# Kernel optimization log

Measured on AMD Instinct MI355X. Metric: run time of the kernel, lower is better.

The kernel has to match this reference:

```python
import jax, jax.numpy as jnp
import numpy as np

D_MODEL = 1024
D_STATE = 16
D_CONV = 4
EXPAND = 2
INNER = EXPAND * D_MODEL          # 2048
DT_RANK = (D_MODEL + 15) // 16     # 64 ('auto' heuristic)
BATCH = 1
SEQLEN = 2048
DT_MIN, DT_MAX, DT_FLOOR = 1e-3, 1e-1, 1e-4


def setup_inputs() -> dict:
    key = jax.random.key(0)
    ks = jax.random.split(key, 8)
    hidden_states = jax.random.normal(ks[0], (BATCH, SEQLEN, D_MODEL), jnp.float32)
    W_in = jax.random.normal(ks[1], (2 * INNER, D_MODEL), jnp.float32) * (D_MODEL ** -0.5)
    conv_w = jax.random.normal(ks[2], (INNER, D_CONV), jnp.float32) * 0.02
    conv_b = jnp.zeros((INNER,), jnp.float32)
    W_x = jax.random.normal(ks[3], (DT_RANK + 2 * D_STATE, INNER), jnp.float32) * (INNER ** -0.5)
    dt_init_std = DT_RANK ** -0.5
    W_dt = jax.random.uniform(ks[4], (INNER, DT_RANK), jnp.float32, -dt_init_std, dt_init_std)
    # dt_bias = inverse-softplus of dt sampled log-uniform in [dt_min, dt_max]
    dt = jnp.exp(jax.random.uniform(ks[5], (INNER,), jnp.float32)
                 * (np.log(DT_MAX) - np.log(DT_MIN)) + np.log(DT_MIN))
    dt = jnp.clip(dt, DT_FLOOR)
    dt_bias = dt + jnp.log(-jnp.expm1(-dt))
    A_log = jax.random.normal(ks[6], (INNER, D_STATE), jnp.float32) * 0.5
    D_skip = jnp.ones((INNER,), jnp.float32)
    W_out = jax.random.normal(ks[7], (D_MODEL, INNER), jnp.float32) * (INNER ** -0.5)
    return dict(hidden_states=hidden_states, W_in=W_in, conv_w=conv_w, conv_b=conv_b,
                W_x=W_x, W_dt=W_dt, dt_bias=dt_bias, A_log=A_log, D_skip=D_skip, W_out=W_out)


def _silu(x):
    return x * jax.nn.sigmoid(x)


def reference(hidden_states, W_in, conv_w, conv_b, W_x, W_dt, dt_bias, A_log, D_skip, W_out):
    # in_proj: (B, L, d_model) -> (B, L, 2*inner), split into x-branch and gate
    xz = hidden_states @ W_in.T
    proj, gate = jnp.split(xz, 2, axis=-1)

    # depthwise causal conv along L with silu activation
    xc = proj.transpose(0, 2, 1)                       # (B, inner, L)
    kernel = conv_w[:, None, :]                        # (inner, 1, d_conv)
    conv = jax.lax.conv_general_dilated(
        xc, kernel, window_strides=(1,), padding=[(D_CONV - 1, 0)],
        dimension_numbers=('NCH', 'OIH', 'NCH'), feature_group_count=INNER)
    conv = _silu(conv + conv_b[None, :, None])         # (B, inner, L)
    u = conv.transpose(0, 2, 1)                        # (B, L, inner)

    # x_proj -> low-rank dt, B, C per-token
    projt = u @ W_x.T                                  # (B, L, dt_rank + 2*N)
    dt_lr, Bp, Cp = jnp.split(projt, [DT_RANK, DT_RANK + D_STATE], axis=-1)
    delta = jax.nn.softplus(dt_lr @ W_dt.T + dt_bias)  # (B, L, inner)

    # selective scan: h_t = exp(delta*A) h_{t-1} + delta*B_t*u_t
    A = -jnp.exp(A_log)                                # (inner, N)
    dA = jnp.exp(jnp.einsum('bld,dn->lbdn', delta, A))            # (L,B,inner,N)
    dBu = jnp.einsum('bld,bln,bld->lbdn', delta, Bp, u)           # (L,B,inner,N)

    def step(h, inp):
        dA_t, dBu_t = inp
        h = dA_t * h + dBu_t
        return h, h

    h0 = jnp.zeros((hidden_states.shape[0], INNER, D_STATE), u.dtype)
    _, hs = jax.lax.scan(step, h0, (dA, dBu))          # (L,B,inner,N)

    y = jnp.einsum('lbdn,bln->bld', hs, Cp)            # (B, L, inner)
    y = y + D_skip * u                                 # D skip connection
    y = y * _silu(gate)                                # gated output
    return y @ W_out.T                                 # (B, L, d_model)
```

## Files before the change

### kernel.cpp

```cpp
#include <hip/hip_runtime.h>
#include <hip/hip_bf16.h>

#define SEQLEN 2048
#define DMODEL 1024
#define INNER  2048
#define DSTATE 16
#define DTRANK 64
#define NPROJ  96
#define NPAD   128
#define CHUNK  16
#define NCH    128
#define KSPLIT 16

typedef __attribute__((ext_vector_type(8))) short bf16x8;
typedef __attribute__((ext_vector_type(4))) float f32x4;

__device__ __forceinline__ float softplusf(float x) {
    return (x > 20.f) ? x : log1pf(__expf(x));
}
__device__ __forceinline__ unsigned short f2bf(float x) {
    unsigned u = __float_as_uint(x);
    return (unsigned short)((u + 0x7FFF + ((u >> 16) & 1)) >> 16);
}
__device__ __forceinline__ float bf2f(unsigned short x) {
    return __uint_as_float((unsigned)x << 16);
}
__device__ __forceinline__ void gload_lds16(const void* g, void* l) {
    __builtin_amdgcn_global_load_lds(
        (__attribute__((address_space(1))) const unsigned int*)g,
        (__attribute__((address_space(3))) unsigned int*)l,
        16, 0, 0);
}
__device__ __forceinline__ void cvt8(const float* __restrict__ in,
                                     unsigned short* __restrict__ out, int i) {
    float4 a = ((const float4*)in)[2 * i];
    float4 b = ((const float4*)in)[2 * i + 1];
    uint4 v;
    v.x = f2bf(a.x) | ((unsigned)f2bf(a.y) << 16);
    v.y = f2bf(a.z) | ((unsigned)f2bf(a.w) << 16);
    v.z = f2bf(b.x) | ((unsigned)f2bf(b.y) << 16);
    v.w = f2bf(b.z) | ((unsigned)f2bf(b.w) << 16);
    ((uint4*)out)[i] = v;
}

__global__ __launch_bounds__(256)
void cvt_all(const float* __restrict__ hidden, const float* __restrict__ W_in,
             const float* __restrict__ W_out, const float* __restrict__ W_dt,
             const float* __restrict__ W_x,
             unsigned short* __restrict__ hid_b, unsigned short* __restrict__ Win_b,
             unsigned short* __restrict__ Wout_b, unsigned short* __restrict__ Wdt_b,
             unsigned short* __restrict__ Wx_b)
{
    int i = blockIdx.x * 256 + threadIdx.x;
    if (i < 262144) { cvt8(hidden, hid_b, i); return; }
    i -= 262144;
    if (i < 524288) { cvt8(W_in, Win_b, i); return; }
    i -= 524288;
    if (i < 262144) { cvt8(W_out, Wout_b, i); return; }
    i -= 262144;
    if (i < 16384)  { cvt8(W_dt, Wdt_b, i); return; }
    i -= 16384;
    if (i < 32768) {
        int row = i >> 8;
        if (row < NPROJ) cvt8(W_x, Wx_b, i);
        else ((uint4*)Wx_b)[i] = make_uint4(0, 0, 0, 0);
    }
}

template<int BM, int BN, int EPI>
__global__ __launch_bounds__(256)
void gemm_bf16(const unsigned short* __restrict__ A, const int lda,
               const unsigned short* __restrict__ B, const int ldb,
               void* __restrict__ Cv, const int ldc, const long long zCstride,
               const int K, const int kspan, const float* __restrict__ bias)
{
    constexpr int FM = BM / 32;
    constexpr int FN = BN / 32;
    __shared__ alignas(16) short As[BM * 64];
    __shared__ alignas(16) short Bs[BN * 64];

    const int tid  = threadIdx.x;
    const int wave = tid >> 6;
    const int lane = tid & 63;

    int bid = blockIdx.y * gridDim.x + blockIdx.x;
    const int q = (gridDim.x * gridDim.y) >> 3;
    bid = (bid & 7) * q + (bid >> 3);
    const int bx = bid % gridDim.x;
    const int by = bid / gridDim.x;

    const long long row0 = (long long)by * BM;
    const long long col0 = (long long)bx * BN;
    const int wm = (wave >> 1) * (BM / 2);
    const int wn = (wave & 1) * (BN / 2);
    const int kstart = blockIdx.z * kspan;
    const int kend   = min(K, kstart + kspan);

    f32x4 acc[FM][FN] = {};

    const int srow   = tid >> 3;
    const int schunk = (tid & 7) ^ (srow & 7);
    const unsigned short* gA = A + (row0 + srow) * lda + schunk * 8;
    const unsigned short* gB = B + (col0 + srow) * ldb + schunk * 8;
    short* lA = &As[srow * 64 + (tid & 7) * 8];
    short* lB = &Bs[srow * 64 + (tid & 7) * 8];

    const int fr = lane & 15;
    const int hi = lane >> 4;
    const int rb = fr & 7;

    for (int kt = kstart; kt < kend; kt += 64) {
#pragma unroll
        for (int r = 0; r < BM; r += 32)
            gload_lds16(gA + (long long)r * lda + kt, lA + r * 64);
#pragma unroll
        for (int r = 0; r < BN; r += 32)
            gload_lds16(gB + (long long)r * ldb + kt, lB + r * 64);
        __syncthreads();

#pragma unroll
        for (int half = 0; half < 2; ++half) {
            const int kc = (((half << 2) + hi) ^ rb) * 8;
            bf16x8 af[FM], bfr[FN];
#pragma unroll
            for (int mi = 0; mi < FM; ++mi)
                af[mi] = *(const bf16x8*)&As[(wm + mi * 16 + fr) * 64 + kc];
#pragma unroll
            for (int ni = 0; ni < FN; ++ni)
                bfr[ni] = *(const bf16x8*)&Bs[(wn + ni * 16 + fr) * 64 + kc];
#pragma unroll
            for (int mi = 0; mi < FM; ++mi)
#pragma unroll
                for (int ni = 0; ni < FN; ++ni)
                    acc[mi][ni] = __builtin_amdgcn_mfma_f32_16x16x32_bf16(
                        af[mi], bfr[ni], acc[mi][ni], 0, 0, 0);
        }
        __syncthreads();
    }

    const int cr = hi * 4;
#pragma unroll
    for (int mi = 0; mi < FM; ++mi)
#pragma unroll
        for (int ni = 0; ni < FN; ++ni) {
            long long rbase = row0 + wm + mi * 16 + cr;
            long long col   = col0 + wn + ni * 16 + fr;
#pragma unroll
            for (int r = 0; r < 4; ++r) {
                long long idx = (rbase + r) * ldc + col;
                if (EPI == 0) {
                    ((float*)Cv)[(long long)blockIdx.z * zCstride + idx] = acc[mi][ni][r];
                } else if (EPI == 1) {
                    ((unsigned short*)Cv)[idx] = f2bf(acc[mi][ni][r]);
                } else {
                    ((unsigned short*)Cv)[idx] = f2bf(softplusf(acc[mi][ni][r] + bias[col]));
                }
            }
        }
}

__global__ __launch_bounds__(256)
void reduce_out(const float* __restrict__ part, float* __restrict__ out)
{
    int i = blockIdx.x * 256 + threadIdx.x;
    float4 a = ((const float4*)part)[i];
    float4 b = ((const float4*)part)[i + SEQLEN * DMODEL / 4];
    a.x += b.x; a.y += b.y; a.z += b.z; a.w += b.w;
    ((float4*)out)[i] = a;
}

__global__ __launch_bounds__(256)
void conv_silu_kernel(const unsigned short* __restrict__ xz_b, const float* __restrict__ cw,
                      const float* __restrict__ cb, unsigned short* __restrict__ u_b)
{
    int i = blockIdx.x * 256 + threadIdx.x;
    int l  = i >> 8;
    int dq = i & 255;
    int d  = dq * 8;
    float4 wv[8];
#pragma unroll
    for (int k = 0; k < 8; ++k) wv[k] = ((const float4*)cw)[d + k];
    float a[8];
    {
        float4 c0 = ((const float4*)cb)[dq * 2];
        float4 c1 = ((const float4*)cb)[dq * 2 + 1];
        a[0] = c0.x; a[1] = c0.y; a[2] = c0.z; a[3] = c0.w;
        a[4] = c1.x; a[5] = c1.y; a[6] = c1.z; a[7] = c1.w;
    }
#pragma unroll
    for (int j = 0; j < 4; ++j) {
        int ls = l - 3 + j;
        if (ls >= 0) {
            bf16x8 x = *(const bf16x8*)&xz_b[(long long)ls * 4096 + d];
#pragma unroll
            for (int k = 0; k < 8; ++k)
                a[k] = fmaf(((const float*)&wv[k])[j],
                            bf2f((unsigned short)x[k]), a[k]);
        }
    }
    uint4 p;
    float r[8];
#pragma unroll
    for (int k = 0; k < 8; ++k) r[k] = a[k] / (1.f + __expf(-a[k]));
    p.x = f2bf(r[0]) | ((unsigned)f2bf(r[1]) << 16);
    p.y = f2bf(r[2]) | ((unsigned)f2bf(r[3]) << 16);
    p.z = f2bf(r[4]) | ((unsigned)f2bf(r[5]) << 16);
    p.w = f2bf(r[6]) | ((unsigned)f2bf(r[7]) << 16);
    ((uint4*)u_b)[i] = p;
}

__global__ __launch_bounds__(256)
void reduce_part(const float* __restrict__ part, float* __restrict__ projt,
                 unsigned short* __restrict__ projt_b)
{
    int i = blockIdx.x * 256 + threadIdx.x;
    float s = 0.f;
#pragma unroll
    for (int z = 0; z < KSPLIT; ++z) s += part[(long long)z * SEQLEN * NPAD + i];
    projt[i] = s;
    projt_b[i] = f2bf(s);
}

__global__ __launch_bounds__(256)
void scan_phase1(const unsigned short* __restrict__ delta_bf,
                 const unsigned short* __restrict__ u_b,
                 const float* __restrict__ projt, const float* __restrict__ A_log,
                 float* __restrict__ Sloc, float* __restrict__ sumd)
{
    __shared__ float Bsh[CHUNK][16];
    const int d  = blockIdx.x * 256 + threadIdx.x;
    const int c  = blockIdx.y;
    const int l0 = c * CHUNK;
    for (int i = threadIdx.x; i < CHUNK * 16; i += 256) {
        int l = i >> 4, j = i & 15;
        Bsh[l][j] = projt[(l0 + l) * NPAD + DTRANK + j];
    }
    __syncthreads();

    float A2[DSTATE];
#pragma unroll
    for (int n = 0; n < DSTATE; ++n)
        A2[n] = -__expf(A_log[d * DSTATE + n]) * 1.4426950408889634f;

    float dl[CHUNK], du[CHUNK];
#pragma unroll
    for (int t = 0; t < CHUNK; ++t) {
        int l = l0 + t;
        float dv = bf2f(delta_bf[l * INNER + d]);
        dl[t] = dv;
        du[t] = dv * bf2f(u_b[l * INNER + d]);
    }

    float h[DSTATE];
#pragma unroll
    for (int n = 0; n < DSTATE; ++n) h[n] = 0.f;
    float sd = 0.f;

#pragma unroll
    for (int t = 0; t < CHUNK; ++t) {
        sd += dl[t];
#pragma unroll
        for (int n = 0; n < DSTATE; ++n) {
            float dA = exp2f(dl[t] * A2[n]);
            h[n] = fmaf(dA, h[n], du[t] * Bsh[t][n]);
        }
    }
#pragma unroll
    for (int n = 0; n < DSTATE; ++n)
        Sloc[(c * INNER + d) * DSTATE + n] = h[n];
    sumd[c * INNER + d] = sd;
}

__global__ __launch_bounds__(256)
void scan_phase2(float* __restrict__ S, const float* __restrict__ sumd,
                 const float* __restrict__ A_log)
{
    int i = blockIdx.x * 256 + threadIdx.x;
    int d = i >> 4;
    float A2 = -__expf(A_log[i]) * 1.4426950408889634f;
    float H = 0.f;
#pragma unroll
    for (int c = 0; c < NCH; ++c) {
        float s = S[c * (INNER * DSTATE) + i];
        float P = exp2f(A2 * sumd[c * INNER + d]);
        S[c * (INNER * DSTATE) + i] = H;
        H = fmaf(P, H, s);
    }
}

__global__ __launch_bounds__(256)
void scan_phase3(const unsigned short* __restrict__ delta_bf,
                 const unsigned short* __restrict__ u_b,
                 const float* __restrict__ projt, const float* __restrict__ A_log,
                 const float* __restrict__ Hinit, const unsigned short* __restrict__ xz_b,
                 const float* __restrict__ D_skip, unsigned short* __restrict__ ybf)
{
    __shared__ float BC[CHUNK][32];
    const int d  = blockIdx.x * 256 + threadIdx.x;
    const int c  = blockIdx.y;
    const int l0 = c * CHUNK;
    for (int i = threadIdx.x; i < CHUNK * 32; i += 256) {
        int l = i >> 5, j = i & 31;
        BC[l][j] = projt[(l0 + l) * NPAD + DTRANK + j];
    }
    __syncthreads();

    float A2[DSTATE];
#pragma unroll
    for (int n = 0; n < DSTATE; ++n)
        A2[n] = -__expf(A_log[d * DSTATE + n]) * 1.4426950408889634f;

    float dl[CHUNK], uv[CHUNK];
#pragma unroll
    for (int t = 0; t < CHUNK; ++t) {
        int l = l0 + t;
        dl[t] = bf2f(delta_bf[l * INNER + d]);
        uv[t] = bf2f(u_b[l * INNER + d]);
    }

    float h[DSTATE];
#pragma unroll
    for (int n = 0; n < DSTATE; ++n)
        h[n] = Hinit[(c * INNER + d) * DSTATE + n];
    const float Dd = D_skip[d];

#pragma unroll
    for (int t = 0; t < CHUNK; ++t) {
        int l = l0 + t;
        float du = dl[t] * uv[t];
        float y = 0.f;
#pragma unroll
        for (int n = 0; n < DSTATE; ++n) {
            float dA = exp2f(dl[t] * A2[n]);
            h[n] = fmaf(dA, h[n], du * BC[t][n]);
            y = fmaf(h[n], BC[t][16 + n], y);
        }
        float yv = fmaf(Dd, uv[t], y);
        float g = bf2f(xz_b[(long long)l * 4096 + 2048 + d]);
        float sg = g / (1.f + __expf(-g));
        ybf[l * INNER + d] = f2bf(yv * sg);
    }
}

extern "C" void kernel_launch(void* const* d_in, const int* in_sizes, int n_in,
                              void* d_out, int out_size, void* d_ws, size_t ws_size,
                              hipStream_t stream)
{
    const float* hidden  = (const float*)d_in[0];
    const float* W_in    = (const float*)d_in[1];
    const float* conv_w  = (const float*)d_in[2];
    const float* conv_b  = (const float*)d_in[3];
    const float* W_x     = (const float*)d_in[4];
    const float* W_dt    = (const float*)d_in[5];
    const float* dt_bias = (const float*)d_in[6];
    const float* A_log   = (const float*)d_in[7];
    const float* D_skip  = (const float*)d_in[8];
    const float* W_out   = (const float*)d_in[9];
    float* out = (float*)d_out;

    char* base = (char*)d_ws;
    unsigned short* xz_b    = (unsigned short*)(base + 0);
    unsigned short* hid_b   = (unsigned short*)(base + 16777216);
    unsigned short* Win_b   = (unsigned short*)(base + 20971520);
    unsigned short* u_b     = (unsigned short*)(base + 16777216);
    float*          part16  = (float*)(base + 25165824);
    float*          Sloc    = (float*)(base + 25165824);
    float*          opart   = (float*)(base + 25165824);
    unsigned short* dlt_b   = (unsigned short*)(base + 41943040);
    unsigned short* y_b     = (unsigned short*)(base + 50331648);
    float*          projt   = (float*)(base + 58720256);
    unsigned short* projt_b = (unsigned short*)(base + 59768832);
    unsigned short* Wout_b  = (unsigned short*)(base + 60293120);
    unsigned short* Wx_b    = (unsigned short*)(base + 64487424);
    unsigned short* Wdt_b   = (unsigned short*)(base + 65011712);
    float*          sumd    = (float*)(base + 65273856);

    cvt_all<<<4289, 256, 0, stream>>>(hidden, W_in, W_out, W_dt, W_x,
                                      hid_b, Win_b, Wout_b, Wdt_b, Wx_b);

    gemm_bf16<128, 128, 1><<<dim3(32, 16, 1), 256, 0, stream>>>(
        hid_b, DMODEL, Win_b, DMODEL, xz_b, 4096, 0, DMODEL, DMODEL, nullptr);

    conv_silu_kernel<<<SEQLEN * 256 / 256, 256, 0, stream>>>(xz_b, conv_w, conv_b, u_b);

    gemm_bf16<128, 128, 0><<<dim3(1, 16, KSPLIT), 256, 0, stream>>>(
        u_b, INNER, Wx_b, INNER, part16, NPAD, (long long)SEQLEN * NPAD,
        INNER, INNER / KSPLIT, nullptr);
    reduce_part<<<SEQLEN * NPAD / 256, 256, 0, stream>>>(part16, projt, projt_b);

    gemm_bf16<128, 64, 2><<<dim3(32, 16, 1), 256, 0, stream>>>(
        projt_b, NPAD, Wdt_b, DTRANK, dlt_b, INNER, 0, DTRANK, DTRANK, dt_bias);

    scan_phase1<<<dim3(INNER / 256, NCH), 256, 0, stream>>>(dlt_b, u_b, projt, A_log, Sloc, sumd);
    scan_phase2<<<(INNER * DSTATE) / 256, 256, 0, stream>>>(Sloc, sumd, A_log);
    scan_phase3<<<dim3(INNER / 256, NCH), 256, 0, stream>>>(dlt_b, u_b, projt, A_log,
                                                            Sloc, xz_b, D_skip, y_b);

    gemm_bf16<128, 64, 0><<<dim3(16, 16, 2), 256, 0, stream>>>(
        y_b, INNER, Wout_b, INNER, opart, DMODEL, (long long)SEQLEN * DMODEL,
        INNER, INNER / 2, nullptr);
    reduce_out<<<SEQLEN * DMODEL / 1024, 256, 0, stream>>>(opart, out);
}
```

Measured before the change: 170.6 us.

## Fuse conv+SiLU into x_proj GEMM prologue and store scan chunk states in bf16

Removes the separate conv_silu kernel by computing the causal depthwise conv and SiLU inside the x_proj split-K GEMM. Each block writes the result into LDS as the A tile and also stores u to global memory for the scan. The chunk-boundary scan states (Sloc) are now stored as bf16 instead of fp32, which halves their traffic across phase1, phase2 and phase3. The cost is lower precision in the inter-chunk state carry, plus extra redundant xz loads for the conv halo inside the GEMM.

```diff
diff --git a/kernel.cpp b/kernel.cpp
--- a/kernel.cpp
+++ b/kernel.cpp
@@ -160,6 +160,118 @@
 }
 
 __global__ __launch_bounds__(256)
+void xproj_fused(const unsigned short* __restrict__ xz_b,
+                 const float* __restrict__ cw, const float* __restrict__ cb,
+                 const unsigned short* __restrict__ Wx_b,
+                 unsigned short* __restrict__ u_b, float* __restrict__ Cv)
+{
+    __shared__ alignas(16) short As[128 * 64];
+    __shared__ alignas(16) short Bs[128 * 64];
+
+    const int tid  = threadIdx.x;
+    const int wave = tid >> 6;
+    const int lane = tid & 63;
+
+    int bid = blockIdx.y;
+    bid = (bid & 7) * 2 + (bid >> 3);
+    const long long row0 = (long long)bid * 128;
+
+    const int wm = (wave >> 1) * 64;
+    const int wn = (wave & 1) * 64;
+    const int kstart = blockIdx.z * (INNER / KSPLIT);
+
+    f32x4 acc[2][2] = {};
+
+    const int srow   = tid >> 3;
+    const int gchunk = (tid & 7) ^ (srow & 7);
+    short* lA = &As[srow * 64 + (tid & 7) * 8];
+    short* lB = &Bs[srow * 64 + (tid & 7) * 8];
+    const unsigned short* gB = Wx_b + srow * INNER + gchunk * 8;
+
+    const int fr = lane & 15;
+    const int hi = lane >> 4;
+    const int rb = fr & 7;
+
+    for (int kt = kstart; kt < kstart + 128; kt += 64) {
+        const int d = kt + gchunk * 8;
+        float4 wv[8];
+#pragma unroll
+        for (int k = 0; k < 8; ++k) wv[k] = ((const float4*)cw)[d + k];
+        float bias8[8];
+        {
+            float4 c0 = ((const float4*)cb)[d >> 2];
+            float4 c1 = ((const float4*)cb)[(d >> 2) + 1];
+            bias8[0] = c0.x; bias8[1] = c0.y; bias8[2] = c0.z; bias8[3] = c0.w;
+            bias8[4] = c1.x; bias8[5] = c1.y; bias8[6] = c1.z; bias8[7] = c1.w;
+        }
+#pragma unroll
+        for (int r = 0; r < 128; r += 32) {
+            const long long l = row0 + srow + r;
+            float a[8];
+#pragma unroll
+            for (int k = 0; k < 8; ++k) a[k] = bias8[k];
+#pragma unroll
+            for (int j = 0; j < 4; ++j) {
+                long long ls = l - 3 + j;
+                if (ls >= 0) {
+                    bf16x8 x = *(const bf16x8*)&xz_b[ls * 4096 + d];
+#pragma unroll
+                    for (int k = 0; k < 8; ++k)
+                        a[k] = fmaf(((const float*)&wv[k])[j],
+                                    bf2f((unsigned short)x[k]), a[k]);
+                }
+            }
+            float s8[8];
+#pragma unroll
+            for (int k = 0; k < 8; ++k) s8[k] = a[k] / (1.f + __expf(-a[k]));
+            uint4 p;
+            p.x = f2bf(s8[0]) | ((unsigned)f2bf(s8[1]) << 16);
+            p.y = f2bf(s8[2]) | ((unsigned)f2bf(s8[3]) << 16);
+            p.z = f2bf(s8[4]) | ((unsigned)f2bf(s8[5]) << 16);
+            p.w = f2bf(s8[6]) | ((unsigned)f2bf(s8[7]) << 16);
+            *(uint4*)(lA + r * 64) = p;
+            *(uint4*)&u_b[l * INNER + d] = p;
+        }
+#pragma unroll
+        for (int r = 0; r < 128; r += 32)
+            gload_lds16(gB + (long long)r * INNER + kt, lB + r * 64);
+        __syncthreads();
+
+#pragma unroll
+        for (int half = 0; half < 2; ++half) {
+            const int kc = (((half << 2) + hi) ^ rb) * 8;
+            bf16x8 af[2], bfr[2];
+#pragma unroll
+            for (int mi = 0; mi < 2; ++mi)
+                af[mi] = *(const bf16x8*)&As[(wm + mi * 16 + fr) * 64 + kc];
+#pragma unroll
+            for (int ni = 0; ni < 2; ++ni)
+                bfr[ni] = *(const bf16x8*)&Bs[(wn + ni * 16 + fr) * 64 + kc];
+#pragma unroll
+            for (int mi = 0; mi < 2; ++mi)
+#pragma unroll
+                for (int ni = 0; ni < 2; ++ni)
+                    acc[mi][ni] = __builtin_amdgcn_mfma_f32_16x16x32_bf16(
+                        af[mi], bfr[ni], acc[mi][ni], 0, 0, 0);
+        }
+        __syncthreads();
+    }
+
+    const int cr = hi * 4;
+#pragma unroll
+    for (int mi = 0; mi < 2; ++mi)
+#pragma unroll
+        for (int ni = 0; ni < 2; ++ni) {
+            long long rbase = row0 + wm + mi * 16 + cr;
+            long long col   = wn + ni * 16 + fr;
+#pragma unroll
+            for (int r = 0; r < 4; ++r)
+                Cv[(long long)blockIdx.z * (SEQLEN * NPAD) +
+                   (rbase + r) * NPAD + col] = acc[mi][ni][r];
+        }
+}
+
+__global__ __launch_bounds__(256)
 void reduce_out(const float* __restrict__ part, float* __restrict__ out)
 {
     int i = blockIdx.x * 256 + threadIdx.x;
@@ -170,46 +282,6 @@
 }
 
 __global__ __launch_bounds__(256)
-void conv_silu_kernel(const unsigned short* __restrict__ xz_b, const float* __restrict__ cw,
-                      const float* __restrict__ cb, unsigned short* __restrict__ u_b)
-{
-    int i = blockIdx.x * 256 + threadIdx.x;
-    int l  = i >> 8;
-    int dq = i & 255;
-    int d  = dq * 8;
-    float4 wv[8];
-#pragma unroll
-    for (int k = 0; k < 8; ++k) wv[k] = ((const float4*)cw)[d + k];
-    float a[8];
-    {
-        float4 c0 = ((const float4*)cb)[dq * 2];
-        float4 c1 = ((const float4*)cb)[dq * 2 + 1];
-        a[0] = c0.x; a[1] = c0.y; a[2] = c0.z; a[3] = c0.w;
-        a[4] = c1.x; a[5] = c1.y; a[6] = c1.z; a[7] = c1.w;
-    }
-#pragma unroll
-    for (int j = 0; j < 4; ++j) {
-        int ls = l - 3 + j;
-        if (ls >= 0) {
-            bf16x8 x = *(const bf16x8*)&xz_b[(long long)ls * 4096 + d];
-#pragma unroll
-            for (int k = 0; k < 8; ++k)
-                a[k] = fmaf(((const float*)&wv[k])[j],
-                            bf2f((unsigned short)x[k]), a[k]);
-        }
-    }
-    uint4 p;
-    float r[8];
-#pragma unroll
-    for (int k = 0; k < 8; ++k) r[k] = a[k] / (1.f + __expf(-a[k]));
-    p.x = f2bf(r[0]) | ((unsigned)f2bf(r[1]) << 16);
-    p.y = f2bf(r[2]) | ((unsigned)f2bf(r[3]) << 16);
-    p.z = f2bf(r[4]) | ((unsigned)f2bf(r[5]) << 16);
-    p.w = f2bf(r[6]) | ((unsigned)f2bf(r[7]) << 16);
-    ((uint4*)u_b)[i] = p;
-}
-
-__global__ __launch_bounds__(256)
 void reduce_part(const float* __restrict__ part, float* __restrict__ projt,
                  unsigned short* __restrict__ projt_b)
 {
@@ -225,7 +297,7 @@
 void scan_phase1(const unsigned short* __restrict__ delta_bf,
                  const unsigned short* __restrict__ u_b,
                  const float* __restrict__ projt, const float* __restrict__ A_log,
-                 float* __restrict__ Sloc, float* __restrict__ sumd)
+                 unsigned short* __restrict__ Slocb, float* __restrict__ sumd)
 {
     __shared__ float Bsh[CHUNK][16];
     const int d  = blockIdx.x * 256 + threadIdx.x;
@@ -265,14 +337,22 @@
             h[n] = fmaf(dA, h[n], du[t] * Bsh[t][n]);
         }
     }
-#pragma unroll
-    for (int n = 0; n < DSTATE; ++n)
-        Sloc[(c * INNER + d) * DSTATE + n] = h[n];
+    uint4 p0, p1;
+    p0.x = f2bf(h[0])  | ((unsigned)f2bf(h[1])  << 16);
+    p0.y = f2bf(h[2])  | ((unsigned)f2bf(h[3])  << 16);
+    p0.z = f2bf(h[4])  | ((unsigned)f2bf(h[5])  << 16);
+    p0.w = f2bf(h[6])  | ((unsigned)f2bf(h[7])  << 16);
+    p1.x = f2bf(h[8])  | ((unsigned)f2bf(h[9])  << 16);
+    p1.y = f2bf(h[10]) | ((unsigned)f2bf(h[11]) << 16);
+    p1.z = f2bf(h[12]) | ((unsigned)f2bf(h[13]) << 16);
+    p1.w = f2bf(h[14]) | ((unsigned)f2bf(h[15]) << 16);
+    uint4* dst = (uint4*)&Slocb[(long long)(c * INNER + d) * DSTATE];
+    dst[0] = p0; dst[1] = p1;
     sumd[c * INNER + d] = sd;
 }
 
 __global__ __launch_bounds__(256)
-void scan_phase2(float* __restrict__ S, const float* __restrict__ sumd,
+void scan_phase2(unsigned short* __restrict__ S, const float* __restrict__ sumd,
                  const float* __restrict__ A_log)
 {
     int i = blockIdx.x * 256 + threadIdx.x;
@@ -281,9 +361,9 @@
     float H = 0.f;
 #pragma unroll
     for (int c = 0; c < NCH; ++c) {
-        float s = S[c * (INNER * DSTATE) + i];
+        float s = bf2f(S[c * (INNER * DSTATE) + i]);
         float P = exp2f(A2 * sumd[c * INNER + d]);
-        S[c * (INNER * DSTATE) + i] = H;
+        S[c * (INNER * DSTATE) + i] = f2bf(H);
         H = fmaf(P, H, s);
     }
 }
@@ -292,7 +372,8 @@
 void scan_phase3(const unsigned short* __restrict__ delta_bf,
                  const unsigned short* __restrict__ u_b,
                  const float* __restrict__ projt, const float* __restrict__ A_log,
-                 const float* __restrict__ Hinit, const unsigned short* __restrict__ xz_b,
+                 const unsigned short* __restrict__ Hinit,
+                 const unsigned short* __restrict__ xz_b,
                  const float* __restrict__ D_skip, unsigned short* __restrict__ ybf)
 {
     __shared__ float BC[CHUNK][32];
@@ -319,9 +400,18 @@
     }
 
     float h[DSTATE];
-#pragma unroll
-    for (int n = 0; n < DSTATE; ++n)
-        h[n] = Hinit[(c * INNER + d) * DSTATE + n];
+    {
+        const uint4* hp = (const uint4*)&Hinit[(long long)(c * INNER + d) * DSTATE];
+        uint4 p0 = hp[0], p1 = hp[1];
+        h[0]  = bf2f((unsigned short)(p0.x & 0xffff)); h[1]  = bf2f((unsigned short)(p0.x >> 16));
+        h[2]  = bf2f((unsigned short)(p0.y & 0xffff)); h[3]  = bf2f((unsigned short)(p0.y >> 16));
+        h[4]  = bf2f((unsigned short)(p0.z & 0xffff)); h[5]  = bf2f((unsigned short)(p0.z >> 16));
+        h[6]  = bf2f((unsigned short)(p0.w & 0xffff)); h[7]  = bf2f((unsigned short)(p0.w >> 16));
+        h[8]  = bf2f((unsigned short)(p1.x & 0xffff)); h[9]  = bf2f((unsigned short)(p1.x >> 16));
+        h[10] = bf2f((unsigned short)(p1.y & 0xffff)); h[11] = bf2f((unsigned short)(p1.y >> 16));
+        h[12] = bf2f((unsigned short)(p1.z & 0xffff)); h[13] = bf2f((unsigned short)(p1.z >> 16));
+        h[14] = bf2f((unsigned short)(p1.w & 0xffff)); h[15] = bf2f((unsigned short)(p1.w >> 16));
+    }
     const float Dd = D_skip[d];
 
 #pragma unroll
@@ -364,7 +454,7 @@
     unsigned short* Win_b   = (unsigned short*)(base + 20971520);
     unsigned short* u_b     = (unsigned short*)(base + 16777216);
     float*          part16  = (float*)(base + 25165824);
-    float*          Sloc    = (float*)(base + 25165824);
+    unsigned short* Slocb   = (unsigned short*)(base + 25165824);
     float*          opart   = (float*)(base + 25165824);
     unsigned short* dlt_b   = (unsigned short*)(base + 41943040);
     unsigned short* y_b     = (unsigned short*)(base + 50331648);
@@ -381,20 +471,17 @@
     gemm_bf16<128, 128, 1><<<dim3(32, 16, 1), 256, 0, stream>>>(
         hid_b, DMODEL, Win_b, DMODEL, xz_b, 4096, 0, DMODEL, DMODEL, nullptr);
 
-    conv_silu_kernel<<<SEQLEN * 256 / 256, 256, 0, stream>>>(xz_b, conv_w, conv_b, u_b);
-
-    gemm_bf16<128, 128, 0><<<dim3(1, 16, KSPLIT), 256, 0, stream>>>(
-        u_b, INNER, Wx_b, INNER, part16, NPAD, (long long)SEQLEN * NPAD,
-        INNER, INNER / KSPLIT, nullptr);
+    xproj_fused<<<dim3(1, 16, KSPLIT), 256, 0, stream>>>(
+        xz_b, conv_w, conv_b, Wx_b, u_b, part16);
     reduce_part<<<SEQLEN * NPAD / 256, 256, 0, stream>>>(part16, projt, projt_b);
 
     gemm_bf16<128, 64, 2><<<dim3(32, 16, 1), 256, 0, stream>>>(
         projt_b, NPAD, Wdt_b, DTRANK, dlt_b, INNER, 0, DTRANK, DTRANK, dt_bias);
 
-    scan_phase1<<<dim3(INNER / 256, NCH), 256, 0, stream>>>(dlt_b, u_b, projt, A_log, Sloc, sumd);
-    scan_phase2<<<(INNER * DSTATE) / 256, 256, 0, stream>>>(Sloc, sumd, A_log);
+    scan_phase1<<<dim3(INNER / 256, NCH), 256, 0, stream>>>(dlt_b, u_b, projt, A_log, Slocb, sumd);
+    scan_phase2<<<(INNER * DSTATE) / 256, 256, 0, stream>>>(Slocb, sumd, A_log);
     scan_phase3<<<dim3(INNER / 256, NCH), 256, 0, stream>>>(dlt_b, u_b, projt, A_log,
-                                                            Sloc, xz_b, D_skip, y_b);
+                                                            Slocb, xz_b, D_skip, y_b);
 
     gemm_bf16<128, 64, 0><<<dim3(16, 16, 2), 256, 0, stream>>>(
         y_b, INNER, Wout_b, INNER, opart, DMODEL, (long long)SEQLEN * DMODEL,
```

After: 161.1 us. 1.06x faster.
